# Optimization experiments

Measured on AMD Instinct MI355X. Metric: run time of the kernel, lower is better.

## Reference

```python
import jax, jax.numpy as jnp
import numpy as np

S_GRID = 14.0
L_COORD = 5.0
L_NOOBJ = 0.5
B = 2


def _xywh2xyxy(b):
    # b: [..., 4] with (x, y, w, h); x,y are divided by S per the original module
    xy = b[..., :2] / S_GRID
    wh = b[..., 2:4]
    return jnp.concatenate([xy - 0.5 * wh, xy + 0.5 * wh], axis=-1)


def setup_inputs() -> dict:
    key = jax.random.key(0)
    k1, k2, k3, k4 = jax.random.split(key, 4)
    N, S, C = 4096, 14, 20
    pred_tensor = jax.random.uniform(k1, (N, S, S, B * 5 + C), dtype=jnp.float32, minval=0.05, maxval=1.0)
    target_boxes = jax.random.uniform(k2, (N, S, S, 4), dtype=jnp.float32, minval=0.05, maxval=1.0)
    target_cls = jax.random.normal(k3, (N, S, S, C), dtype=jnp.float32)
    has_object_map = jax.random.randint(k4, (N, S, S), 0, 2).astype(jnp.bool_)
    return {"pred_tensor": pred_tensor, "target_boxes": target_boxes,
            "target_cls": target_cls, "has_object_map": has_object_map}


def reference(pred_tensor, target_boxes, target_cls, has_object_map):
    N = pred_tensor.shape[0]
    mask = has_object_map                      # [N,S,S] bool
    maskf = mask.astype(pred_tensor.dtype)
    pb = pred_tensor[..., :B * 5].reshape(*pred_tensor.shape[:3], B, 5)  # [N,S,S,B,5]
    pc = pred_tensor[..., B * 5:]              # [N,S,S,20]

    # class loss: masked sum of squared errors over classes
    cls_loss = jnp.sum(maskf * jnp.sum((target_cls - pc) ** 2, axis=-1))

    # no-object loss: conf^2 on cells without objects, summed over both boxes
    conf = pb[..., 4]                          # [N,S,S,B]
    no_obj_loss = L_NOOBJ * jnp.sum(jnp.where(~mask[..., None], conf, 0.0) ** 2)

    # per-cell IoU of target vs each of the B predicted boxes (diag of original NxM)
    t_xyxy = _xywh2xyxy(target_boxes)          # [N,S,S,4]
    p_xyxy = _xywh2xyxy(pb[..., :4])           # [N,S,S,B,4]
    lt = jnp.maximum(t_xyxy[..., None, :2], p_xyxy[..., :2])
    rb = jnp.minimum(t_xyxy[..., None, 2:], p_xyxy[..., 2:])
    wh = jnp.clip(rb - lt, 0.0)
    inter = wh[..., 0] * wh[..., 1]            # [N,S,S,B]
    area_t = (t_xyxy[..., 2] - t_xyxy[..., 0]) * (t_xyxy[..., 3] - t_xyxy[..., 1])
    area_p = (p_xyxy[..., 2] - p_xyxy[..., 0]) * (p_xyxy[..., 3] - p_xyxy[..., 1])
    iou = inter / (area_t[..., None] + area_p - inter)  # [N,S,S,B]

    best_iou = jnp.max(iou, axis=-1)           # [N,S,S]
    best_idx = jnp.argmax(iou, axis=-1)        # [N,S,S]
    best_box = jnp.take_along_axis(pb, best_idx[..., None, None], axis=3)[..., 0, :]  # [N,S,S,5]

    xy_diff = jnp.where(mask[..., None], best_box[..., :2] - target_boxes[..., :2], 0.0)
    wh_p = jnp.where(mask[..., None], best_box[..., 2:4], 1.0)
    wh_t = jnp.where(mask[..., None], target_boxes[..., 2:4], 1.0)
    reg_loss = L_COORD * (jnp.sum(xy_diff ** 2)
                          + jnp.sum((jnp.sqrt(wh_p) - jnp.sqrt(wh_t)) ** 2))

    # containing-object confidence loss: mse(best_iou, best_box_conf) on object cells
    containing_obj_loss = jnp.sum(jnp.where(mask, best_iou - best_box[..., 4], 0.0) ** 2)

    total_loss = (cls_loss + no_obj_loss + reg_loss + containing_obj_loss) / N
    return (total_loss, reg_loss, containing_obj_loss, no_obj_loss, cls_loss)
```

## Files before the change

kernel.cpp:

```cpp
#include <hip/hip_runtime.h>
#include <math.h>


#define BLOCK 256
#define WPB 4
#define CPW 64

__global__ __launch_bounds__(BLOCK) void k_yolo(
    const float*  __restrict__ pred,
    const float4* __restrict__ tbox4,
    const float4* __restrict__ tcls4,
    const int*    __restrict__ mask,
    float4*       __restrict__ partial,
    int n_cells)
{
    __shared__ float sp[WPB][CPW * 30];
    const int tid  = threadIdx.x;
    const int lane = tid & 63;
    const int w    = tid >> 6;
    const long long cell0 = ((long long)blockIdx.x * WPB + w) * CPW;

    float cls = 0.f, noobj = 0.f, reg = 0.f, cont = 0.f;

    int mflag = 0;
    if (cell0 < n_cells) {
        const float4* p4 = reinterpret_cast<const float4*>(pred + cell0 * 30);
        float4* s4 = reinterpret_cast<float4*>(sp[w]);
        #pragma unroll
        for (int i = 0; i < 8; ++i) {
            int k = lane + i * 64;
            if (k < 480) s4[k] = p4[k];
        }
        long long cell = cell0 + lane;
        if (cell < (long long)n_cells) mflag = mask[cell];
    }
    __syncthreads();

    if (cell0 + lane < (long long)n_cells) {
        const float2* pc2 = reinterpret_cast<const float2*>(sp[w] + lane * 30);
        float2 v0 = pc2[0], v1 = pc2[1], v2 = pc2[2], v3 = pc2[3], v4 = pc2[4];
        float4 tb = tbox4[cell0 + lane];
        if (mflag) {
            float txc = tb.x / 14.0f, tyc = tb.y / 14.0f;
            float t0 = txc - 0.5f * tb.z, t1 = tyc - 0.5f * tb.w;
            float t2 = txc + 0.5f * tb.z, t3 = tyc + 0.5f * tb.w;
            float area_t = (t2 - t0) * (t3 - t1);
            float bx[2] = { v0.x, v2.y }, by[2] = { v0.y, v3.x };
            float bw[2] = { v1.x, v3.y }, bh[2] = { v1.y, v4.x };
            float bcf[2] = { v2.x, v4.y };
            float iou[2];
            #pragma unroll
            for (int b = 0; b < 2; ++b) {
                float px = bx[b] / 14.0f, py = by[b] / 14.0f;
                float q0 = px - 0.5f * bw[b], q1 = py - 0.5f * bh[b];
                float q2 = px + 0.5f * bw[b], q3 = py + 0.5f * bh[b];
                float lt0 = fmaxf(t0, q0), lt1 = fmaxf(t1, q1);
                float rb0 = fminf(t2, q2), rb1 = fminf(t3, q3);
                float ww = fmaxf(rb0 - lt0, 0.f), hh = fmaxf(rb1 - lt1, 0.f);
                float inter = ww * hh;
                float area_p = (q2 - q0) * (q3 - q1);
                iou[b] = inter / (area_t + area_p - inter);
            }
            int bi = (iou[1] > iou[0]) ? 1 : 0;
            float dx = bx[bi] - tb.x, dy = by[bi] - tb.y;
            float swd = sqrtf(bw[bi]) - sqrtf(tb.z);
            float shd = sqrtf(bh[bi]) - sqrtf(tb.w);
            reg = 5.0f * (dx*dx + dy*dy + swd*swd + shd*shd);
            float dco = iou[bi] - bcf[bi];
            cont = dco * dco;
        } else {
            noobj = 0.5f * (v2.x * v2.x + v4.y * v4.y);
        }
    }

    if (cell0 < n_cells) {
        const float4* t4 = tcls4 + cell0 * 5;
        #pragma unroll
        for (int i = 0; i < 5; ++i) {
            int j = lane + i * 64;
            int c = j / 5;
            int q = j - 5 * c;
            int mc = __shfl(mflag, c, 64);
            if (mc) {
                float4 t = t4[j];
                const float2* s2 = reinterpret_cast<const float2*>(sp[w] + c * 30 + 10 + q * 4);
                float2 a = s2[0], b = s2[1];
                float d0 = t.x - a.x, d1 = t.y - a.y;
                float d2 = t.z - b.x, d3 = t.w - b.y;
                cls += d0*d0 + d1*d1 + d2*d2 + d3*d3;
            }
        }
    }

    #pragma unroll
    for (int off = 32; off; off >>= 1) {
        cls   += __shfl_down(cls,   off, 64);
        noobj += __shfl_down(noobj, off, 64);
        reg   += __shfl_down(reg,   off, 64);
        cont  += __shfl_down(cont,  off, 64);
    }
    __shared__ float4 swr[WPB];
    if (lane == 0) swr[w] = make_float4(cls, noobj, reg, cont);
    __syncthreads();
    if (tid == 0) {
        float4 a = swr[0];
        #pragma unroll
        for (int i = 1; i < WPB; ++i) {
            float4 b = swr[i];
            a.x += b.x; a.y += b.y; a.z += b.z; a.w += b.w;
        }
        partial[blockIdx.x] = a;
    }
}

__global__ __launch_bounds__(BLOCK) void k_final(
    const float4* __restrict__ partial, int nblocks,
    float* __restrict__ out, float invN)
{
    float4 acc = make_float4(0.f, 0.f, 0.f, 0.f);
    for (int b = threadIdx.x; b < nblocks; b += BLOCK) {
        float4 v = partial[b];
        acc.x += v.x; acc.y += v.y; acc.z += v.z; acc.w += v.w;
    }
    #pragma unroll
    for (int off = 32; off; off >>= 1) {
        acc.x += __shfl_down(acc.x, off, 64);
        acc.y += __shfl_down(acc.y, off, 64);
        acc.z += __shfl_down(acc.z, off, 64);
        acc.w += __shfl_down(acc.w, off, 64);
    }
    __shared__ float4 sw[WPB];
    int lane = threadIdx.x & 63, w = threadIdx.x >> 6;
    if (lane == 0) sw[w] = acc;
    __syncthreads();
    if (threadIdx.x == 0) {
        float cls = 0.f, noobj = 0.f, reg = 0.f, cont = 0.f;
        #pragma unroll
        for (int i = 0; i < WPB; ++i) {
            cls += sw[i].x; noobj += sw[i].y; reg += sw[i].z; cont += sw[i].w;
        }
        out[0] = (cls + noobj + reg + cont) * invN;
        out[1] = reg;
        out[2] = cont;
        out[3] = noobj;
        out[4] = cls;
    }
}

extern "C" void kernel_launch(void* const* d_in, const int* in_sizes, int n_in,
                              void* d_out, int out_size, void* d_ws, size_t ws_size,
                              hipStream_t stream) {
    const float*  pred  = (const float*)d_in[0];
    const float4* tbox4 = (const float4*)d_in[1];
    const float4* tcls4 = (const float4*)d_in[2];
    const int*    mask  = (const int*)d_in[3];
    float* out = (float*)d_out;
    float4* partial = (float4*)d_ws;

    int n_cells = in_sizes[3];
    int N = in_sizes[0] / (14 * 14 * 30);
    int nblocks = (n_cells + BLOCK - 1) / BLOCK;

    hipLaunchKernelGGL(k_yolo, dim3(nblocks), dim3(BLOCK), 0, stream,
                       pred, tbox4, tcls4, mask, partial, n_cells);
    hipLaunchKernelGGL(k_final, dim3(1), dim3(BLOCK), 0, stream,
                       partial, nblocks, out, 1.0f / (float)N);
}
```

Before: 201.3 us.

## Stream pred as float2 and fuse class loss into load loop, shrink LDS

Each wave now reads its pred slice as coalesced float2 words. Box words go into a smaller per-wave LDS buffer, and class words are compared directly against target_cls in registers. The block-wide __syncthreads is replaced by an lgkmcnt wait plus a sched barrier, and launch bounds request 8 blocks per CU. This drops the full 30-float LDS staging and the second class pass, cutting LDS traffic and raising occupancy. The cost is narrower float2 global loads with per-element division and modulo index maths, plus a reliance on wave-local LDS visibility with no block barrier.

```diff
diff --git a/kernel.cpp b/kernel.cpp
--- a/kernel.cpp
+++ b/kernel.cpp
@@ -6,45 +6,66 @@
 #define WPB 4
 #define CPW 64
 
-__global__ __launch_bounds__(BLOCK) void k_yolo(
+__global__ __launch_bounds__(BLOCK, 8) void k_yolo(
     const float*  __restrict__ pred,
     const float4* __restrict__ tbox4,
-    const float4* __restrict__ tcls4,
+    const float2* __restrict__ tcls2,
     const int*    __restrict__ mask,
     float4*       __restrict__ partial,
     int n_cells)
 {
-    __shared__ float sp[WPB][CPW * 30];
+    __shared__ float2 sbox[WPB][CPW * 5];
     const int tid  = threadIdx.x;
     const int lane = tid & 63;
     const int w    = tid >> 6;
     const long long cell0 = ((long long)blockIdx.x * WPB + w) * CPW;
 
+    long long rem = (long long)n_cells - cell0;
+    int lim = rem < 0 ? 0 : (rem > CPW ? CPW : (int)rem);
+
     float cls = 0.f, noobj = 0.f, reg = 0.f, cont = 0.f;
 
     int mflag = 0;
-    if (cell0 < n_cells) {
-        const float4* p4 = reinterpret_cast<const float4*>(pred + cell0 * 30);
-        float4* s4 = reinterpret_cast<float4*>(sp[w]);
-        #pragma unroll
-        for (int i = 0; i < 8; ++i) {
-            int k = lane + i * 64;
-            if (k < 480) s4[k] = p4[k];
+    float4 tb = make_float4(0.f, 0.f, 0.f, 0.f);
+    if (lane < lim) {
+        mflag = mask[cell0 + lane];
+        tb    = tbox4[cell0 + lane];
+    }
+
+    const float2* p2  = reinterpret_cast<const float2*>(pred) + cell0 * 15;
+    const float2* t2  = tcls2 + cell0 * 10;
+    float2*       sb2 = sbox[w];
+
+    #pragma unroll
+    for (int k = 0; k < 15; ++k) {
+        int j = lane + (k << 6);
+        int c = j / 15;
+        int r = j - c * 15;
+        int mc = __shfl(mflag, c, 64);
+        if (c < lim) {
+            float2 v = p2[j];
+            if (r < 5) {
+                sb2[c * 5 + r] = v;
+            } else if (mc) {
+                float2 t = t2[c * 10 + (r - 5)];
+                float d0 = t.x - v.x, d1 = t.y - v.y;
+                cls = fmaf(d0, d0, cls);
+                cls = fmaf(d1, d1, cls);
+            }
         }
-        long long cell = cell0 + lane;
-        if (cell < (long long)n_cells) mflag = mask[cell];
     }
-    __syncthreads();
 
-    if (cell0 + lane < (long long)n_cells) {
-        const float2* pc2 = reinterpret_cast<const float2*>(sp[w] + lane * 30);
-        float2 v0 = pc2[0], v1 = pc2[1], v2 = pc2[2], v3 = pc2[3], v4 = pc2[4];
-        float4 tb = tbox4[cell0 + lane];
+    asm volatile("s_waitcnt lgkmcnt(0)" ::: "memory");
+    __builtin_amdgcn_sched_barrier(0);
+
+    if (lane < lim) {
+        const float2* bl = sb2 + lane * 5;
+        float2 v0 = bl[0], v1 = bl[1], v2 = bl[2], v3 = bl[3], v4 = bl[4];
         if (mflag) {
             float txc = tb.x / 14.0f, tyc = tb.y / 14.0f;
             float t0 = txc - 0.5f * tb.z, t1 = tyc - 0.5f * tb.w;
-            float t2 = txc + 0.5f * tb.z, t3 = tyc + 0.5f * tb.w;
-            float area_t = (t2 - t0) * (t3 - t1);
+            float t2c = txc + 0.5f * tb.z, t3 = tyc + 0.5f * tb.w;
+            float area_t = (t2c - t0) * (t3 - t1);
             float bx[2] = { v0.x, v2.y }, by[2] = { v0.y, v3.x };
             float bw[2] = { v1.x, v3.y }, bh[2] = { v1.y, v4.x };
             float bcf[2] = { v2.x, v4.y };
@@ -55,7 +76,7 @@
                 float q0 = px - 0.5f * bw[b], q1 = py - 0.5f * bh[b];
                 float q2 = px + 0.5f * bw[b], q3 = py + 0.5f * bh[b];
                 float lt0 = fmaxf(t0, q0), lt1 = fmaxf(t1, q1);
-                float rb0 = fminf(t2, q2), rb1 = fminf(t3, q3);
+                float rb0 = fminf(t2c, q2), rb1 = fminf(t3, q3);
                 float ww = fmaxf(rb0 - lt0, 0.f), hh = fmaxf(rb1 - lt1, 0.f);
                 float inter = ww * hh;
                 float area_p = (q2 - q0) * (q3 - q1);
@@ -70,25 +91,6 @@
             cont = dco * dco;
         } else {
             noobj = 0.5f * (v2.x * v2.x + v4.y * v4.y);
-        }
-    }
-
-    if (cell0 < n_cells) {
-        const float4* t4 = tcls4 + cell0 * 5;
-        #pragma unroll
-        for (int i = 0; i < 5; ++i) {
-            int j = lane + i * 64;
-            int c = j / 5;
-            int q = j - 5 * c;
-            int mc = __shfl(mflag, c, 64);
-            if (mc) {
-                float4 t = t4[j];
-                const float2* s2 = reinterpret_cast<const float2*>(sp[w] + c * 30 + 10 + q * 4);
-                float2 a = s2[0], b = s2[1];
-                float d0 = t.x - a.x, d1 = t.y - a.y;
-                float d2 = t.z - b.x, d3 = t.w - b.y;
-                cls += d0*d0 + d1*d1 + d2*d2 + d3*d3;
-            }
         }
     }
 
@@ -152,7 +154,7 @@
                               hipStream_t stream) {
     const float*  pred  = (const float*)d_in[0];
     const float4* tbox4 = (const float4*)d_in[1];
-    const float4* tcls4 = (const float4*)d_in[2];
+    const float2* tcls2 = (const float2*)d_in[2];
     const int*    mask  = (const int*)d_in[3];
     float* out = (float*)d_out;
     float4* partial = (float4*)d_ws;
@@ -162,7 +164,7 @@
     int nblocks = (n_cells + BLOCK - 1) / BLOCK;
 
     hipLaunchKernelGGL(k_yolo, dim3(nblocks), dim3(BLOCK), 0, stream,
-                       pred, tbox4, tcls4, mask, partial, n_cells);
+                       pred, tbox4, tcls2, mask, partial, n_cells);
     hipLaunchKernelGGL(k_final, dim3(1), dim3(BLOCK), 0, stream,
                        partial, nblocks, out, 1.0f / (float)N);
 }
```

After: 207.3 us. 1.03x slower.

## Use persistent double-buffered global_load_lds pipeline for YOLO loss kernel

Applied to the files above, without the earlier changes.

Replaces the one-tile-per-wave launch with a fixed grid of persistent waves that stride over 64-cell tiles. Prediction tiles are loaded straight into LDS with global_load_lds into two buffers, with manual vmcnt waits, so the next tile's load overlaps the current tile's math. Mask, box and class targets are prefetched into registers one tile ahead, and the class loss is now computed per cell instead of via shuffles. The handwritten waitcnt counts and sched barriers are fragile, and the extra register use may lower occupancy.

```diff
diff --git a/kernel.cpp b/kernel.cpp
--- a/kernel.cpp
+++ b/kernel.cpp
@@ -2,9 +2,97 @@
 #include <math.h>
 
 
-#define BLOCK 256
-#define WPB 4
-#define CPW 64
+#define BLOCK 128
+#define WPB 2
+#define CPT 64
+#define NBLK 1280
+
+#define DMA_TILE(buf, tile) do {                                              \
+    const __attribute__((address_space(1))) float4* gp_ =                     \
+        (const __attribute__((address_space(1))) float4*)(pred) + (size_t)(tile) * 480; \
+    __attribute__((address_space(3))) float4* lp_ =                           \
+        (__attribute__((address_space(3))) float4*)(buf);                     \
+    _Pragma("unroll")                                                         \
+    for (int i_ = 0; i_ < 7; ++i_)                                            \
+        __builtin_amdgcn_global_load_lds(                                     \
+            (const __attribute__((address_space(1))) void*)(gp_ + lane + i_ * 64), \
+            (__attribute__((address_space(3))) void*)(lp_ + i_ * 64), 16, 0, 0); \
+    if (lane < 32)                                                            \
+        __builtin_amdgcn_global_load_lds(                                     \
+            (const __attribute__((address_space(1))) void*)(gp_ + 448 + lane),\
+            (__attribute__((address_space(3))) void*)(lp_ + 448), 16, 0, 0);  \
+} while (0)
+
+#define LOAD_SCAL(tile, mf, tbv, tcv) do {                                    \
+    long long c_ = (long long)(tile) * CPT + lane;                            \
+    mf  = mask[c_];                                                           \
+    tbv = tbox4[c_];                                                          \
+    const float4* t4_ = tcls4 + c_ * 5;                                       \
+    tcv[0] = t4_[0]; tcv[1] = t4_[1]; tcv[2] = t4_[2];                        \
+    tcv[3] = t4_[3]; tcv[4] = t4_[4];                                         \
+} while (0)
+
+#define LDSREAD(buf)                                                          \
+    const float2* pc2_ = reinterpret_cast<const float2*>((buf) + lane * 30);  \
+    float2 v0 = pc2_[0],  v1 = pc2_[1],  v2 = pc2_[2],  v3 = pc2_[3],  v4 = pc2_[4];  \
+    float2 v5 = pc2_[5],  v6 = pc2_[6],  v7 = pc2_[7],  v8 = pc2_[8],  v9 = pc2_[9];  \
+    float2 v10 = pc2_[10], v11 = pc2_[11], v12 = pc2_[12], v13 = pc2_[13], v14 = pc2_[14];
+
+#define CELLMATH(mf, tbv, tcv) do {                                           \
+    if (mf) {                                                                 \
+        float txc = tbv.x / 14.0f, tyc = tbv.y / 14.0f;                       \
+        float t0 = txc - 0.5f * tbv.z, t1 = tyc - 0.5f * tbv.w;               \
+        float t2c = txc + 0.5f * tbv.z, t3 = tyc + 0.5f * tbv.w;              \
+        float area_t = (t2c - t0) * (t3 - t1);                                \
+        float bx[2] = { v0.x, v2.y }, by[2] = { v0.y, v3.x };                 \
+        float bw[2] = { v1.x, v3.y }, bh[2] = { v1.y, v4.x };                 \
+        float bcf[2] = { v2.x, v4.y };                                        \
+        float iou[2];                                                         \
+        _Pragma("unroll")                                                     \
+        for (int b_ = 0; b_ < 2; ++b_) {                                      \
+            float px = bx[b_] / 14.0f, py = by[b_] / 14.0f;                   \
+            float q0 = px - 0.5f * bw[b_], q1 = py - 0.5f * bh[b_];           \
+            float q2 = px + 0.5f * bw[b_], q3 = py + 0.5f * bh[b_];           \
+            float lt0 = fmaxf(t0, q0), lt1 = fmaxf(t1, q1);                   \
+            float rb0 = fminf(t2c, q2), rb1 = fminf(t3, q3);                  \
+            float ww = fmaxf(rb0 - lt0, 0.f), hh = fmaxf(rb1 - lt1, 0.f);     \
+            float inter = ww * hh;                                            \
+            float area_p = (q2 - q0) * (q3 - q1);                             \
+            iou[b_] = inter / (area_t + area_p - inter);                      \
+        }                                                                     \
+        int bi = (iou[1] > iou[0]) ? 1 : 0;           \
+        float dx = bx[bi] - tbv.x, dy = by[bi] - tbv.y;                       \
+        float swd = sqrtf(bw[bi]) - sqrtf(tbv.z);                             \
+        float shd = sqrtf(bh[bi]) - sqrtf(tbv.w);                             \
+        reg = fmaf(5.0f, dx*dx + dy*dy + swd*swd + shd*shd, reg);             \
+        float dco = iou[bi] - bcf[bi];                                        \
+        cont = fmaf(dco, dco, cont);                                          \
+        float d_;                                                             \
+        d_ = tcv[0].x - v5.x;  cls = fmaf(d_, d_, cls);                       \
+        d_ = tcv[0].y - v5.y;  cls = fmaf(d_, d_, cls);                       \
+        d_ = tcv[0].z - v6.x;  cls = fmaf(d_, d_, cls);                       \
+        d_ = tcv[0].w - v6.y;  cls = fmaf(d_, d_, cls);                       \
+        d_ = tcv[1].x - v7.x;  cls = fmaf(d_, d_, cls);                       \
+        d_ = tcv[1].y - v7.y;  cls = fmaf(d_, d_, cls);                       \
+        d_ = tcv[1].z - v8.x;  cls = fmaf(d_, d_, cls);                       \
+        d_ = tcv[1].w - v8.y;  cls = fmaf(d_, d_, cls);                       \
+        d_ = tcv[2].x - v9.x;  cls = fmaf(d_, d_, cls);                       \
+        d_ = tcv[2].y - v9.y;  cls = fmaf(d_, d_, cls);                       \
+        d_ = tcv[2].z - v10.x; cls = fmaf(d_, d_, cls);                       \
+        d_ = tcv[2].w - v10.y; cls = fmaf(d_, d_, cls);                       \
+        d_ = tcv[3].x - v11.x; cls = fmaf(d_, d_, cls);                       \
+        d_ = tcv[3].y - v11.y; cls = fmaf(d_, d_, cls);                       \
+        d_ = tcv[3].z - v12.x; cls = fmaf(d_, d_, cls);                       \
+        d_ = tcv[3].w - v12.y; cls = fmaf(d_, d_, cls);                       \
+        d_ = tcv[4].x - v13.x; cls = fmaf(d_, d_, cls);                       \
+        d_ = tcv[4].y - v13.y; cls = fmaf(d_, d_, cls);                       \
+        d_ = tcv[4].z - v14.x; cls = fmaf(d_, d_, cls);                       \
+        d_ = tcv[4].w - v14.y; cls = fmaf(d_, d_, cls);                       \
+    } else {                                                                  \
+        noobj = fmaf(0.5f * v2.x, v2.x, noobj);                               \
+        noobj = fmaf(0.5f * v4.y, v4.y, noobj);                               \
+    }                                                                         \
+} while (0)
 
 __global__ __launch_bounds__(BLOCK) void k_yolo(
     const float*  __restrict__ pred,
@@ -14,81 +102,79 @@
     float4*       __restrict__ partial,
     int n_cells)
 {
-    __shared__ float sp[WPB][CPW * 30];
+    __shared__ float sp[WPB][2][CPT * 30];
     const int tid  = threadIdx.x;
     const int lane = tid & 63;
     const int w    = tid >> 6;
-    const long long cell0 = ((long long)blockIdx.x * WPB + w) * CPW;
+
+    const int gw = blockIdx.x * WPB + w;
+    const int GW = gridDim.x * WPB;
+    const int F  = n_cells / CPT;
+    int m = (F > gw) ? ((F - gw - 1) / GW + 1) : 0;
 
     float cls = 0.f, noobj = 0.f, reg = 0.f, cont = 0.f;
 
-    int mflag = 0;
-    if (cell0 < n_cells) {
-        const float4* p4 = reinterpret_cast<const float4*>(pred + cell0 * 30);
-        float4* s4 = reinterpret_cast<float4*>(sp[w]);
-        #pragma unroll
-        for (int i = 0; i < 8; ++i) {
-            int k = lane + i * 64;
-            if (k < 480) s4[k] = p4[k];
-        }
-        long long cell = cell0 + lane;
-        if (cell < (long long)n_cells) mflag = mask[cell];
-    }
-    __syncthreads();
-
-    if (cell0 + lane < (long long)n_cells) {
-        const float2* pc2 = reinterpret_cast<const float2*>(sp[w] + lane * 30);
-        float2 v0 = pc2[0], v1 = pc2[1], v2 = pc2[2], v3 = pc2[3], v4 = pc2[4];
-        float4 tb = tbox4[cell0 + lane];
-        if (mflag) {
-            float txc = tb.x / 14.0f, tyc = tb.y / 14.0f;
-            float t0 = txc - 0.5f * tb.z, t1 = tyc - 0.5f * tb.w;
-            float t2 = txc + 0.5f * tb.z, t3 = tyc + 0.5f * tb.w;
-            float area_t = (t2 - t0) * (t3 - t1);
-            float bx[2] = { v0.x, v2.y }, by[2] = { v0.y, v3.x };
-            float bw[2] = { v1.x, v3.y }, bh[2] = { v1.y, v4.x };
-            float bcf[2] = { v2.x, v4.y };
-            float iou[2];
-            #pragma unroll
-            for (int b = 0; b < 2; ++b) {
-                float px = bx[b] / 14.0f, py = by[b] / 14.0f;
-                float q0 = px - 0.5f * bw[b], q1 = py - 0.5f * bh[b];
-                float q2 = px + 0.5f * bw[b], q3 = py + 0.5f * bh[b];
-                float lt0 = fmaxf(t0, q0), lt1 = fmaxf(t1, q1);
-                float rb0 = fminf(t2, q2), rb1 = fminf(t3, q3);
-                float ww = fmaxf(rb0 - lt0, 0.f), hh = fmaxf(rb1 - lt1, 0.f);
-                float inter = ww * hh;
-                float area_p = (q2 - q0) * (q3 - q1);
-                iou[b] = inter / (area_t + area_p - inter);
+    float* bufA = &sp[w][0][0];
+    float* bufB = &sp[w][1][0];
+
+    int    mf0 = 0, mf1 = 0;
+    float4 tb0 = make_float4(0,0,0,0), tb1 = make_float4(0,0,0,0);
+    float4 tc0[5], tc1[5];
+
+    if (m > 0) {
+        DMA_TILE(bufA, gw);
+        LOAD_SCAL(gw, mf0, tb0, tc0);
+        __builtin_amdgcn_sched_barrier(0);
+        if (m > 1) DMA_TILE(bufB, (long long)gw + GW);
+
+        int k = 0;
+        long long tcur = gw;
+        while (true) {
+            {
+                if (k + 1 < m) asm volatile("s_waitcnt vmcnt(8)" ::: "memory");
+                else           asm volatile("s_waitcnt vmcnt(0)" ::: "memory");
+                __builtin_amdgcn_sched_barrier(0);
+                LDSREAD(bufA)
+                asm volatile("s_waitcnt lgkmcnt(0)" ::: "memory");
+                __builtin_amdgcn_sched_barrier(0);
+                if (k + 1 < m) LOAD_SCAL(tcur + GW, mf1, tb1, tc1);
+                __builtin_amdgcn_sched_barrier(0);
+                if (k + 2 < m) DMA_TILE(bufA, tcur + 2 * GW);
+                CELLMATH(mf0, tb0, tc0);
             }
-            int bi = (iou[1] > iou[0]) ? 1 : 0;
-            float dx = bx[bi] - tb.x, dy = by[bi] - tb.y;
-            float swd = sqrtf(bw[bi]) - sqrtf(tb.z);
-            float shd = sqrtf(bh[bi]) - sqrtf(tb.w);
-            reg = 5.0f * (dx*dx + dy*dy + swd*swd + shd*shd);
-            float dco = iou[bi] - bcf[bi];
-            cont = dco * dco;
-        } else {
-            noobj = 0.5f * (v2.x * v2.x + v4.y * v4.y);
-        }
-    }
-
-    if (cell0 < n_cells) {
-        const float4* t4 = tcls4 + cell0 * 5;
-        #pragma unroll
-        for (int i = 0; i < 5; ++i) {
-            int j = lane + i * 64;
-            int c = j / 5;
-            int q = j - 5 * c;
-            int mc = __shfl(mflag, c, 64);
-            if (mc) {
-                float4 t = t4[j];
-                const float2* s2 = reinterpret_cast<const float2*>(sp[w] + c * 30 + 10 + q * 4);
-                float2 a = s2[0], b = s2[1];
-                float d0 = t.x - a.x, d1 = t.y - a.y;
-                float d2 = t.z - b.x, d3 = t.w - b.y;
-                cls += d0*d0 + d1*d1 + d2*d2 + d3*d3;
+            ++k; tcur += GW;
+            if (k == m) break;
+            {
+                if (k + 1 < m) asm volatile("s_waitcnt vmcnt(8)" ::: "memory");
+                else           asm volatile("s_waitcnt vmcnt(0)" ::: "memory");
+                __builtin_amdgcn_sched_barrier(0);
+                LDSREAD(bufB)
+                asm volatile("s_waitcnt lgkmcnt(0)" ::: "memory");
+                __builtin_amdgcn_sched_barrier(0);
+                if (k + 1 < m) LOAD_SCAL(tcur + GW, mf0, tb0, tc0);
+                __builtin_amdgcn_sched_barrier(0);
+                if (k + 2 < m) DMA_TILE(bufB, tcur + 2 * GW);
+                CELLMATH(mf1, tb1, tc1);
             }
+            ++k; tcur += GW;
+            if (k == m) break;
+        }
+    }
+
+    int rem = n_cells - F * CPT;
+    if (rem > 0 && gw == 0) {
+        long long cell0 = (long long)F * CPT;
+        const float* gsrc = pred + cell0 * 30;
+        for (int kk = lane; kk < rem * 30; kk += 64) bufA[kk] = gsrc[kk];
+        int    mfp = 0;
+        float4 tbp = make_float4(0,0,0,0);
+        float4 tcp[5];
+        if (lane < rem) LOAD_SCAL(F, mfp, tbp, tcp);
+        asm volatile("s_waitcnt vmcnt(0) lgkmcnt(0)" ::: "memory");
+        __builtin_amdgcn_sched_barrier(0);
+        if (lane < rem) {
+            LDSREAD(bufA)
+            CELLMATH(mfp, tbp, tcp);
         }
     }
 
@@ -113,12 +199,12 @@
     }
 }
 
-__global__ __launch_bounds__(BLOCK) void k_final(
+__global__ __launch_bounds__(256) void k_final(
     const float4* __restrict__ partial, int nblocks,
     float* __restrict__ out, float invN)
 {
     float4 acc = make_float4(0.f, 0.f, 0.f, 0.f);
-    for (int b = threadIdx.x; b < nblocks; b += BLOCK) {
+    for (int b = threadIdx.x; b < nblocks; b += 256) {
         float4 v = partial[b];
         acc.x += v.x; acc.y += v.y; acc.z += v.z; acc.w += v.w;
     }
@@ -129,14 +215,14 @@
         acc.z += __shfl_down(acc.z, off, 64);
         acc.w += __shfl_down(acc.w, off, 64);
     }
-    __shared__ float4 sw[WPB];
+    __shared__ float4 sw[4];
     int lane = threadIdx.x & 63, w = threadIdx.x >> 6;
     if (lane == 0) sw[w] = acc;
     __syncthreads();
     if (threadIdx.x == 0) {
         float cls = 0.f, noobj = 0.f, reg = 0.f, cont = 0.f;
         #pragma unroll
-        for (int i = 0; i < WPB; ++i) {
+        for (int i = 0; i < 4; ++i) {
             cls += sw[i].x; noobj += sw[i].y; reg += sw[i].z; cont += sw[i].w;
         }
         out[0] = (cls + noobj + reg + cont) * invN;
@@ -159,10 +245,9 @@
 
     int n_cells = in_sizes[3];
     int N = in_sizes[0] / (14 * 14 * 30);
-    int nblocks = (n_cells + BLOCK - 1) / BLOCK;
-
-    hipLaunchKernelGGL(k_yolo, dim3(nblocks), dim3(BLOCK), 0, stream,
+
+    hipLaunchKernelGGL(k_yolo, dim3(NBLK), dim3(BLOCK), 0, stream,
                        pred, tbox4, tcls4, mask, partial, n_cells);
-    hipLaunchKernelGGL(k_final, dim3(1), dim3(BLOCK), 0, stream,
-                       partial, nblocks, out, 1.0f / (float)N);
+    hipLaunchKernelGGL(k_final, dim3(1), dim3(256), 0, stream,
+                       partial, NBLK, out, 1.0f / (float)N);
 }
```

New measurement: 203.9 us. No clear change (+1.3%).
